# Optimization experiments

Measured on AMD Instinct MI355X. Metric: run time of the kernel, lower is better.

Reference implementation:

```python
import jax, jax.numpy as jnp
import numpy as np

B, N, D = 256, 128, 512
NUM_TYPES, NUM_STATS = 6, 8
W_TYPE, W_STATS, W_CORR = 1.0, 1.0, 0.5
LN_EPS = 1e-5


def setup_inputs() -> dict:
    key = jax.random.key(0)
    ks = jax.random.split(key, 20)
    s = 1.0 / np.sqrt(D)
    inp = {
        "column_embeddings": jax.random.normal(ks[0], (B, N, D), jnp.float32),
        "masked_columns": jax.random.bernoulli(ks[1], 0.15, (B, N)),
        "type_targets": jax.random.randint(ks[2], (N,), 0, NUM_TYPES),
        "column_statistics": jax.random.normal(ks[3], (B, N, NUM_STATS), jnp.float32),
        "column_correlations": jnp.tanh(jax.random.normal(ks[4], (B, N, N), jnp.float32)),
        # type head: Linear(D,D) -> GELU -> LayerNorm -> Linear(D,NUM_TYPES)
        "t_W1": jax.random.normal(ks[5], (D, D), jnp.float32) * s,
        "t_b1": jnp.zeros((D,), jnp.float32),
        "t_g": jnp.ones((D,), jnp.float32),
        "t_beta": jnp.zeros((D,), jnp.float32),
        "t_W2": jax.random.normal(ks[6], (D, NUM_TYPES), jnp.float32) * s,
        "t_b2": jnp.zeros((NUM_TYPES,), jnp.float32),
        # stats head
        "s_W1": jax.random.normal(ks[7], (D, D), jnp.float32) * s,
        "s_b1": jnp.zeros((D,), jnp.float32),
        "s_g": jnp.ones((D,), jnp.float32),
        "s_beta": jnp.zeros((D,), jnp.float32),
        "s_W2": jax.random.normal(ks[8], (D, NUM_STATS), jnp.float32) * s,
        "s_b2": jnp.zeros((NUM_STATS,), jnp.float32),
        # bilinear correlation: x_i^T W x_j + b
        "c_W": jax.random.normal(ks[9], (D, D), jnp.float32) * s,
        "c_b": jnp.zeros((), jnp.float32),
    }
    return inp


def _mlp_head(x, W1, b1, g, beta, W2, b2):
    h = jax.nn.gelu(x @ W1 + b1, approximate=False)
    mu = h.mean(-1, keepdims=True)
    var = ((h - mu) ** 2).mean(-1, keepdims=True)
    h = (h - mu) * jax.lax.rsqrt(var + LN_EPS) * g + beta
    return h @ W2 + b2


def _forward(column_embeddings, masked_columns, type_targets,
             column_statistics, column_correlations,
             t_W1, t_b1, t_g, t_beta, t_W2, t_b2,
             s_W1, s_b1, s_g, s_beta, s_W2, s_b2,
             c_W, c_b):
    e = column_embeddings  # [B,N,D]
    type_logits = _mlp_head(e, t_W1, t_b1, t_g, t_beta, t_W2, t_b2)   # [B,N,T]
    stats_preds = _mlp_head(e, s_W1, s_b1, s_g, s_beta, s_W2, s_b2)   # [B,N,S]

    # batched bilinear correlation: tanh(e_i W e_j + b), diag forced to 1
    u = jnp.einsum('bnd,de->bne', e, c_W)            # [B,N,D]
    corr = jnp.tanh(jnp.einsum('bne,bme->bnm', u, e) + c_b)  # [B,N,N]
    eye = jnp.eye(e.shape[1], dtype=corr.dtype)
    corr = corr * (1.0 - eye) + eye

    m = masked_columns.astype(jnp.float32)           # [B,N]
    n_masked = jnp.maximum(m.sum(), 1.0)

    # type loss: masked-mean cross entropy; targets broadcast over batch
    logp = jax.nn.log_softmax(type_logits, axis=-1)
    tgt = jnp.broadcast_to(type_targets[None, :], m.shape)
    ce = -jnp.take_along_axis(logp, tgt[..., None], axis=-1)[..., 0]  # [B,N]
    type_loss = (ce * m).sum() / n_masked

    # stats loss: masked-mean MSE over [B,N,S]
    se = (stats_preds - column_statistics) ** 2
    stats_loss = (se * m[..., None]).sum() / (n_masked * se.shape[-1])

    # correlation loss: mask_expanded = m_i | m_j
    me = jnp.maximum(m[:, :, None], m[:, None, :])   # [B,N,N]
    n_me = jnp.maximum(me.sum(), 1.0)
    ce2 = (corr - column_correlations) ** 2
    correlation_loss = (ce2 * me).sum() / n_me

    total = W_TYPE * type_loss + W_STATS * stats_loss + W_CORR * correlation_loss
    return total


def reference(column_embeddings, masked_columns, type_targets,
              column_statistics, column_correlations,
              t_W1, t_b1, t_g, t_beta, t_W2, t_b2,
              s_W1, s_b1, s_g, s_beta, s_W2, s_b2,
              c_W, c_b):
    return _forward(column_embeddings, masked_columns, type_targets,
                    column_statistics, column_correlations,
                    t_W1, t_b1, t_g, t_beta, t_W2, t_b2,
                    s_W1, s_b1, s_g, s_beta, s_W2, s_b2,
                    c_W, c_b)
```

## Files before the change

### kernel.cpp

```cpp
#include <hip/hip_runtime.h>
#include <math.h>

#define Bx 256
#define Nx 128
#define Dx 512
#define Mx (Bx * Nx)
#define NTYPES 6
#define NSTATS 8
#define LN_EPS 1e-5f
#define CAP 8192

typedef __attribute__((ext_vector_type(8))) short frag8;
typedef __attribute__((ext_vector_type(4))) float f32x4;

__device__ __forceinline__ unsigned short f2bf(float f) {
    unsigned u = __float_as_uint(f);
    u += 0x7fff + ((u >> 16) & 1);
    return (unsigned short)(u >> 16);
}
__device__ __forceinline__ float bf2f(unsigned short s) {
    return __uint_as_float((unsigned)s << 16);
}

#define ASYNC16(g, l) __builtin_amdgcn_global_load_lds(                      \
    (const __attribute__((address_space(1))) void*)(g),                      \
    (__attribute__((address_space(3))) void*)(l), 16, 0, 0)

#define EB_OFF    0ULL
#define U_OFF     33554432ULL
#define EC_OFF    67108864ULL
#define HC_OFF    75497472ULL
#define WT_OFF    92274688ULL
#define WTC_OFF   93323264ULL
#define LIST_OFF  93847552ULL
#define POS_OFF   93978624ULL
#define CNTS_OFF  94109696ULL
#define PACC_OFF  94110720ULL
#define PCORR_OFF 94112768ULL
#define CNTP_OFF  94113792ULL

__global__ __launch_bounds__(256) void k_prep(
    const float* __restrict__ W0, const float* __restrict__ W1,
    const float* __restrict__ W2, unsigned short* __restrict__ Tcmb,
    unsigned short* __restrict__ Tc, const int* __restrict__ m,
    int* __restrict__ list, int* __restrict__ pos, int* __restrict__ cnts,
    int* cntp) {
    if (blockIdx.x >= 768) {
        const int b = blockIdx.x - 768;
        const int t = threadIdx.x;
        const int r = b * Nx + t;
        int v = 0;
        if (t < 128) v = (m[r] != 0) ? 1 : 0;
        const unsigned long long bal = __ballot(v);
        const int wid = t >> 6, lane = t & 63;
        __shared__ int wcnt[2];
        __shared__ int base;
        if (lane == 0 && wid < 2) wcnt[wid] = __popcll(bal);
        __syncthreads();
        const int cnt = wcnt[0] + wcnt[1];
        if (t == 0) {
            base = atomicAdd(cntp, cnt);
            cnts[b] = cnt;
        }
        __syncthreads();
        if (t < 128) {
            int p = -1;
            if (v) {
                const int rank = __popcll(bal & ((1ULL << lane) - 1)) +
                                 (wid ? wcnt[0] : 0);
                p = base + rank;
                if (p < CAP) list[p] = r;
            }
            pos[r] = (p >= 0 && p < CAP) ? p : -1;
        }
        return;
    }
    const int lin = blockIdx.x * 256 + threadIdx.x;
    const int mid = lin >> 16;
    const int i4  = (lin & 65535) * 4;
    const int n = i4 >> 9, k = i4 & 511;
    const float* W = (mid == 0) ? W0 : (mid == 1) ? W1 : W2;
    unsigned short* T = (mid == 2) ? Tc : (Tcmb + mid * 262144);
    unsigned short o[4];
#pragma unroll
    for (int j = 0; j < 4; ++j) o[j] = f2bf(W[(k + j) * Dx + n]);
    uint2 u;
    u.x = (unsigned)o[0] | ((unsigned)o[1] << 16);
    u.y = (unsigned)o[2] | ((unsigned)o[3] << 16);
    *(uint2*)(T + i4) = u;
}

__global__ __launch_bounds__(256) void k_convE_gather(
    const float* __restrict__ e, const int* __restrict__ pos,
    unsigned short* __restrict__ Eb, unsigned short* __restrict__ Ec) {
    const int r = blockIdx.x * 4 + (threadIdx.x >> 6);
    const int lane = threadIdx.x & 63;
    const int p = pos[r];
    const float4* src = (const float4*)(e + (size_t)r * Dx);
    const float4 a = src[lane * 2];
    const float4 b = src[lane * 2 + 1];
    unsigned short u[8] = {f2bf(a.x), f2bf(a.y), f2bf(a.z), f2bf(a.w),
                           f2bf(b.x), f2bf(b.y), f2bf(b.z), f2bf(b.w)};
    const uint4 v = *(const uint4*)u;
    ((uint4*)(Eb + (size_t)r * Dx))[lane] = v;
    if (p >= 0) ((uint4*)(Ec + (size_t)p * Dx))[lane] = v;
}

__global__ __launch_bounds__(256) void k_gemms(
    const unsigned short* __restrict__ Eb,
    const unsigned short* __restrict__ Ec,
    const unsigned short* __restrict__ Wtc,
    const unsigned short* __restrict__ Wtcmb,
    const float* __restrict__ bias0, const float* __restrict__ bias1,
    unsigned short* __restrict__ U, unsigned short* __restrict__ Hc,
    const int* __restrict__ cntp) {
    __shared__ unsigned short As[128 * 32];
    __shared__ unsigned short Bs[128 * 32];
    const int bid = blockIdx.x;
    const unsigned short *A, *Bt;
    unsigned short* C;
    int row0, col0, ldc, head;
    if (bid < 1024) {
        A = Eb; Bt = Wtc; C = U;
        row0 = (bid >> 2) << 7; col0 = (bid & 3) << 7;
        ldc = 512; head = 0;
    } else {
        const int b2 = bid - 1024;
        row0 = (b2 >> 3) << 7;
        if (row0 >= min(*cntp, CAP)) return;
        col0 = (b2 & 7) << 7;
        A = Ec; Bt = Wtcmb; C = Hc;
        ldc = 1024; head = 1;
    }
    const int t = threadIdx.x;
    const int w = t >> 6, l = t & 63;
    const int wr = (w >> 1) * 64, wcol = (w & 1) * 64;
    const int quad = l >> 4, mr = l & 15;

    const unsigned short* Ag0 = A + (size_t)(row0 + (t >> 2)) * Dx + (t & 3) * 8;
    const unsigned short* Ag1 = Ag0 + (size_t)64 * Dx;
    const unsigned short* Bg0 = Bt + (size_t)(col0 + (t >> 2)) * Dx + (t & 3) * 8;
    const unsigned short* Bg1 = Bg0 + (size_t)64 * Dx;
    unsigned short* Al0 = As + t * 8;
    unsigned short* Al1 = As + (t + 256) * 8;
    unsigned short* Bl0 = Bs + t * 8;
    unsigned short* Bl1 = Bs + (t + 256) * 8;

    f32x4 acc[4][4] = {};
    for (int k0 = 0; k0 < Dx; k0 += 32) {
        __syncthreads();
        ASYNC16(Ag0 + k0, Al0);
        ASYNC16(Ag1 + k0, Al1);
        ASYNC16(Bg0 + k0, Bl0);
        ASYNC16(Bg1 + k0, Bl1);
        __syncthreads();
        frag8 a[4], b[4];
#pragma unroll
        for (int i = 0; i < 4; ++i)
            a[i] = *(const frag8*)&As[(wr + i * 16 + mr) * 32 + quad * 8];
#pragma unroll
        for (int j = 0; j < 4; ++j)
            b[j] = *(const frag8*)&Bs[(wcol + j * 16 + mr) * 32 + quad * 8];
#pragma unroll
        for (int i = 0; i < 4; ++i)
#pragma unroll
            for (int j = 0; j < 4; ++j)
                acc[i][j] = __builtin_amdgcn_mfma_f32_16x16x32_bf16(
                    a[i], b[j], acc[i][j], 0, 0, 0);
    }
#pragma unroll
    for (int i = 0; i < 4; ++i)
#pragma unroll
        for (int j = 0; j < 4; ++j)
#pragma unroll
            for (int r = 0; r < 4; ++r) {
                const int row = row0 + wr + i * 16 + quad * 4 + r;
                const int col = col0 + wcol + j * 16 + mr;
                float v = acc[i][j][r];
                if (head) {
                    v += (col < 512) ? bias0[col] : bias1[col - 512];
                    v = 0.5f * v * (1.0f + erff(v * 0.70710678118654752f));
                }
                C[(size_t)row * ldc + col] = f2bf(v);
            }
}

__global__ __launch_bounds__(256) void k_tail(
    const unsigned short* __restrict__ U,
    const unsigned short* __restrict__ Eb,
    const float* __restrict__ Ct, const int* __restrict__ m,
    const float* __restrict__ cbp, float* __restrict__ pcorr,
    const unsigned short* __restrict__ Hc,
    const float* __restrict__ tg, const float* __restrict__ tbeta,
    const float* __restrict__ tW2, const float* __restrict__ tb2,
    const float* __restrict__ sg, const float* __restrict__ sbeta,
    const float* __restrict__ sW2, const float* __restrict__ sb2,
    const int* __restrict__ list, const int* __restrict__ cntp,
    const int* __restrict__ tgt, const float* __restrict__ stats,
    float* __restrict__ pacc) {
    __shared__ unsigned short As[128 * 32];
    __shared__ unsigned short Bs[128 * 32];
    __shared__ float mloc[128];
    __shared__ float redf[4][2];
    const int t = threadIdx.x;
    const int w = t >> 6, l = t & 63;

    if (blockIdx.x < 256) {
        const int b = blockIdx.x;
        const int wr = (w >> 1) * 64, wcol = (w & 1) * 64;
        const int quad = l >> 4, mr = l & 15;
        if (t < 128) mloc[t] = (m[b * Nx + t] != 0) ? 1.0f : 0.0f;

        const unsigned short* Ub = U + (size_t)b * Nx * Dx;
        const unsigned short* E  = Eb + (size_t)b * Nx * Dx;
        const unsigned short* Ag0 = Ub + (size_t)(t >> 2) * Dx + (t & 3) * 8;
        const unsigned short* Ag1 = Ag0 + (size_t)64 * Dx;
        const unsigned short* Bg0 = E + (size_t)(t >> 2) * Dx + (t & 3) * 8;
        const unsigned short* Bg1 = Bg0 + (size_t)64 * Dx;
        unsigned short* Al0 = As + t * 8;
        unsigned short* Al1 = As + (t + 256) * 8;
        unsigned short* Bl0 = Bs + t * 8;
        unsigned short* Bl1 = Bs + (t + 256) * 8;

        f32x4 acc_r[4][4] = {};
        for (int k0 = 0; k0 < Dx; k0 += 32) {
            __syncthreads();
            ASYNC16(Ag0 + k0, Al0);
            ASYNC16(Ag1 + k0, Al1);
            ASYNC16(Bg0 + k0, Bl0);
            ASYNC16(Bg1 + k0, Bl1);
            __syncthreads();
            frag8 a[4], bfr[4];
#pragma unroll
            for (int i = 0; i < 4; ++i)
                a[i] = *(const frag8*)&As[(wr + i * 16 + mr) * 32 + quad * 8];
#pragma unroll
            for (int j = 0; j < 4; ++j)
                bfr[j] = *(const frag8*)&Bs[(wcol + j * 16 + mr) * 32 + quad * 8];
#pragma unroll
            for (int i = 0; i < 4; ++i)
#pragma unroll
                for (int j = 0; j < 4; ++j)
                    acc_r[i][j] = __builtin_amdgcn_mfma_f32_16x16x32_bf16(
                        a[i], bfr[j], acc_r[i][j], 0, 0, 0);
        }
        const float cb = cbp[0];
        float lsum = 0.0f;
#pragma unroll
        for (int i = 0; i < 4; ++i)
#pragma unroll
            for (int j = 0; j < 4; ++j)
#pragma unroll
                for (int r = 0; r < 4; ++r) {
                    const int row = wr + i * 16 + quad * 4 + r;
                    const int col = wcol + j * 16 + mr;
                    float c = (row == col) ? 1.0f : tanhf(acc_r[i][j][r] + cb);
                    const float me = fmaxf(mloc[row], mloc[col]);
                    const float d = c - Ct[((size_t)b * Nx + row) * Nx + col];
                    lsum += me * d * d;
                }
#pragma unroll
        for (int off = 32; off > 0; off >>= 1) lsum += __shfl_down(lsum, off);
        if (l == 0) redf[w][0] = lsum;
        __syncthreads();
        if (t == 0) pcorr[b] = redf[0][0] + redf[1][0] + redf[2][0] + redf[3][0];
        return;
    }

    const int blk = blockIdx.x - 256;
    const int cnt = min(*cntp, CAP);
    float ce_acc = 0.0f, sse_acc = 0.0f;
    for (int idx = blk * 4 + w; idx < cnt; idx += 256 * 4) {
        const int r = list[idx];
        const uint4 ut = ((const uint4*)(Hc + (size_t)idx * 1024))[l];
        const uint4 us = ((const uint4*)(Hc + (size_t)idx * 1024 + 512))[l];
        float a[8], b8[8];
        {
            const unsigned uu[4] = {ut.x, ut.y, ut.z, ut.w};
            const unsigned vv[4] = {us.x, us.y, us.z, us.w};
#pragma unroll
            for (int j = 0; j < 4; ++j) {
                a[2 * j]      = bf2f((unsigned short)(uu[j] & 0xffff));
                a[2 * j + 1]  = bf2f((unsigned short)(uu[j] >> 16));
                b8[2 * j]     = bf2f((unsigned short)(vv[j] & 0xffff));
                b8[2 * j + 1] = bf2f((unsigned short)(vv[j] >> 16));
            }
        }
        float st = 0, qt = 0, ss = 0, qs = 0;
#pragma unroll
        for (int j = 0; j < 8; ++j) {
            st += a[j]; qt += a[j] * a[j];
            ss += b8[j]; qs += b8[j] * b8[j];
        }
#pragma unroll
        for (int off = 32; off > 0; off >>= 1) {
            st += __shfl_xor(st, off); qt += __shfl_xor(qt, off);
            ss += __shfl_xor(ss, off); qs += __shfl_xor(qs, off);
        }
        const float mt = st * (1.0f / Dx);
        const float rt = rsqrtf(qt * (1.0f / Dx) - mt * mt + LN_EPS);
        const float ms = ss * (1.0f / Dx);
        const float rs = rsqrtf(qs * (1.0f / Dx) - ms * ms + LN_EPS);

        const int c0 = l * 8;
        float tp[6] = {}, sp[8] = {};
#pragma unroll
        for (int j = 0; j < 8; ++j) {
            const int c = c0 + j;
            const float nt = (a[j] - mt) * rt * tg[c] + tbeta[c];
#pragma unroll
            for (int k = 0; k < 6; ++k) tp[k] += nt * tW2[c * 6 + k];
            const float ns = (b8[j] - ms) * rs * sg[c] + sbeta[c];
#pragma unroll
            for (int k = 0; k < 8; ++k) sp[k] += ns * sW2[c * 8 + k];
        }
#pragma unroll
        for (int k = 0; k < 6; ++k)
#pragma unroll
            for (int off = 32; off > 0; off >>= 1) tp[k] += __shfl_down(tp[k], off);
#pragma unroll
        for (int k = 0; k < 8; ++k)
#pragma unroll
            for (int off = 32; off > 0; off >>= 1) sp[k] += __shfl_down(sp[k], off);

        if (l == 0) {
            float lg[6];
#pragma unroll
            for (int k = 0; k < 6; ++k) lg[k] = tp[k] + tb2[k];
            float mx = lg[0];
#pragma unroll
            for (int k = 1; k < 6; ++k) mx = fmaxf(mx, lg[k]);
            float se = 0.0f;
#pragma unroll
            for (int k = 0; k < 6; ++k) se += expf(lg[k] - mx);
            ce_acc += -(lg[tgt[r & (Nx - 1)]] - mx - logf(se));
            float sse = 0.0f;
#pragma unroll
            for (int k = 0; k < 8; ++k) {
                const float d = sp[k] + sb2[k] - stats[(size_t)r * NSTATS + k];
                sse += d * d;
            }
            sse_acc += sse;
        }
    }
    if (l == 0) { redf[w][0] = ce_acc; redf[w][1] = sse_acc; }
    __syncthreads();
    if (t == 0) {
        pacc[2 * blk]     = redf[0][0] + redf[1][0] + redf[2][0] + redf[3][0];
        pacc[2 * blk + 1] = redf[0][1] + redf[1][1] + redf[2][1] + redf[3][1];
    }
}

__global__ __launch_bounds__(256) void k_final(
    const float* __restrict__ pacc, const float* __restrict__ pcorr,
    const int* __restrict__ cnts, const int* __restrict__ cntp,
    float* __restrict__ out) {
    const int t = threadIdx.x, w = t >> 6, lane = t & 63;
    float ce = pacc[2 * t], sse = pacc[2 * t + 1], co = pcorr[t];
    const int c = cnts[t];
    float me = (float)(Nx * Nx) - (float)((Nx - c) * (Nx - c));
#pragma unroll
    for (int off = 32; off > 0; off >>= 1) {
        ce += __shfl_down(ce, off);
        sse += __shfl_down(sse, off);
        co += __shfl_down(co, off);
        me += __shfl_down(me, off);
    }
    __shared__ float red[4][4];
    if (lane == 0) {
        red[w][0] = ce; red[w][1] = sse; red[w][2] = co; red[w][3] = me;
    }
    __syncthreads();
    if (t == 0) {
        const float CE = red[0][0] + red[1][0] + red[2][0] + red[3][0];
        const float SSE = red[0][1] + red[1][1] + red[2][1] + red[3][1];
        const float CO = red[0][2] + red[1][2] + red[2][2] + red[3][2];
        const float ME = red[0][3] + red[1][3] + red[2][3] + red[3][3];
        const float nm = fmaxf((float)*cntp, 1.0f);
        const float nme = fmaxf(ME, 1.0f);
        out[0] = CE / nm + SSE / (nm * (float)NSTATS) + 0.5f * CO / nme;
    }
}

extern "C" void kernel_launch(void* const* d_in, const int* in_sizes, int n_in,
                              void* d_out, int out_size, void* d_ws, size_t ws_size,
                              hipStream_t stream) {
    const float* e      = (const float*)d_in[0];
    const int*   mcols  = (const int*)d_in[1];
    const int*   ttgt   = (const int*)d_in[2];
    const float* stats  = (const float*)d_in[3];
    const float* corrT  = (const float*)d_in[4];
    const float* tW1    = (const float*)d_in[5];
    const float* tb1    = (const float*)d_in[6];
    const float* tg     = (const float*)d_in[7];
    const float* tbeta  = (const float*)d_in[8];
    const float* tW2    = (const float*)d_in[9];
    const float* tb2    = (const float*)d_in[10];
    const float* sW1    = (const float*)d_in[11];
    const float* sb1    = (const float*)d_in[12];
    const float* sg     = (const float*)d_in[13];
    const float* sbeta  = (const float*)d_in[14];
    const float* sW2    = (const float*)d_in[15];
    const float* sb2    = (const float*)d_in[16];
    const float* cW     = (const float*)d_in[17];
    const float* cb     = (const float*)d_in[18];
    float* out = (float*)d_out;

    char* ws = (char*)d_ws;
    unsigned short* Eb    = (unsigned short*)(ws + EB_OFF);
    unsigned short* U     = (unsigned short*)(ws + U_OFF);
    unsigned short* Ec    = (unsigned short*)(ws + EC_OFF);
    unsigned short* Hc    = (unsigned short*)(ws + HC_OFF);
    unsigned short* Wtcmb = (unsigned short*)(ws + WT_OFF);
    unsigned short* Wtc   = (unsigned short*)(ws + WTC_OFF);
    int*   list  = (int*)(ws + LIST_OFF);
    int*   pos   = (int*)(ws + POS_OFF);
    int*   cnts  = (int*)(ws + CNTS_OFF);
    float* pacc  = (float*)(ws + PACC_OFF);
    float* pcorr = (float*)(ws + PCORR_OFF);
    int*   cntp  = (int*)(ws + CNTP_OFF);

    hipMemsetAsync(cntp, 0, sizeof(int), stream);
    k_prep<<<1024, 256, 0, stream>>>(tW1, sW1, cW, Wtcmb, Wtc, mcols,
                                     list, pos, cnts, cntp);
    k_convE_gather<<<Mx / 4, 256, 0, stream>>>(e, pos, Eb, Ec);
    k_gemms<<<1536, 256, 0, stream>>>(Eb, Ec, Wtc, Wtcmb, tb1, sb1, U, Hc, cntp);
    k_tail<<<512, 256, 0, stream>>>(U, Eb, corrT, mcols, cb, pcorr,
                                    Hc, tg, tbeta, tW2, tb2, sg, sbeta, sW2, sb2,
                                    list, cntp, ttgt, stats, pacc);
    k_final<<<1, 256, 0, stream>>>(pacc, pcorr, cnts, cntp, out);
}
```

Baseline: 254.1 us.

## Fuse E conversion into prep, gather masked rows in GEMM, double K-step

```diff
diff --git a/kernel.cpp b/kernel.cpp
--- a/kernel.cpp
+++ b/kernel.cpp
@@ -28,26 +28,25 @@
 
 #define EB_OFF    0ULL
 #define U_OFF     33554432ULL
-#define EC_OFF    67108864ULL
-#define HC_OFF    75497472ULL
-#define WT_OFF    92274688ULL
-#define WTC_OFF   93323264ULL
-#define LIST_OFF  93847552ULL
-#define POS_OFF   93978624ULL
-#define CNTS_OFF  94109696ULL
-#define PACC_OFF  94110720ULL
-#define PCORR_OFF 94112768ULL
-#define CNTP_OFF  94113792ULL
+#define HC_OFF    67108864ULL
+#define WT_OFF    83886080ULL
+#define WTC_OFF   84934656ULL
+#define LIST_OFF  85458944ULL
+#define CNTS_OFF  85590016ULL
+#define PACC_OFF  85591040ULL
+#define PCORR_OFF 85593088ULL
+#define CNTP_OFF  85594112ULL
 
 __global__ __launch_bounds__(256) void k_prep(
-    const float* __restrict__ W0, const float* __restrict__ W1,
-    const float* __restrict__ W2, unsigned short* __restrict__ Tcmb,
+    const float* __restrict__ e, const float* __restrict__ W0,
+    const float* __restrict__ W1, const float* __restrict__ W2,
+    unsigned short* __restrict__ Eb, unsigned short* __restrict__ Tcmb,
     unsigned short* __restrict__ Tc, const int* __restrict__ m,
-    int* __restrict__ list, int* __restrict__ pos, int* __restrict__ cnts,
-    int* cntp) {
-    if (blockIdx.x >= 768) {
-        const int b = blockIdx.x - 768;
-        const int t = threadIdx.x;
+    int* __restrict__ list, int* __restrict__ cnts, int* cntp) {
+    const int bid = blockIdx.x;
+    const int t = threadIdx.x;
+    if (bid < 256) {
+        const int b = bid;
         const int r = b * Nx + t;
         int v = 0;
         if (t < 128) v = (m[r] != 0) ? 1 : 0;
@@ -63,110 +62,106 @@
             cnts[b] = cnt;
         }
         __syncthreads();
-        if (t < 128) {
-            int p = -1;
-            if (v) {
-                const int rank = __popcll(bal & ((1ULL << lane) - 1)) +
-                                 (wid ? wcnt[0] : 0);
-                p = base + rank;
-                if (p < CAP) list[p] = r;
-            }
-            pos[r] = (p >= 0 && p < CAP) ? p : -1;
+        if (t < 128 && v) {
+            const int rank = __popcll(bal & ((1ULL << lane) - 1)) +
+                             (wid ? wcnt[0] : 0);
+            const int p = base + rank;
+            if (p < CAP) list[p] = r;
         }
         return;
     }
-    const int lin = blockIdx.x * 256 + threadIdx.x;
-    const int mid = lin >> 16;
-    const int i4  = (lin & 65535) * 4;
-    const int n = i4 >> 9, k = i4 & 511;
-    const float* W = (mid == 0) ? W0 : (mid == 1) ? W1 : W2;
-    unsigned short* T = (mid == 2) ? Tc : (Tcmb + mid * 262144);
-    unsigned short o[4];
-#pragma unroll
-    for (int j = 0; j < 4; ++j) o[j] = f2bf(W[(k + j) * Dx + n]);
-    uint2 u;
-    u.x = (unsigned)o[0] | ((unsigned)o[1] << 16);
-    u.y = (unsigned)o[2] | ((unsigned)o[3] << 16);
-    *(uint2*)(T + i4) = u;
-}
-
-__global__ __launch_bounds__(256) void k_convE_gather(
-    const float* __restrict__ e, const int* __restrict__ pos,
-    unsigned short* __restrict__ Eb, unsigned short* __restrict__ Ec) {
-    const int r = blockIdx.x * 4 + (threadIdx.x >> 6);
-    const int lane = threadIdx.x & 63;
-    const int p = pos[r];
+    if (bid < 1024) {
+        const int lin = (bid - 256) * 256 + t;
+        const int mid = lin >> 16;
+        const int i4  = (lin & 65535) * 4;
+        const int n = i4 >> 9, k = i4 & 511;
+        const float* W = (mid == 0) ? W0 : (mid == 1) ? W1 : W2;
+        unsigned short* T = (mid == 2) ? Tc : (Tcmb + mid * 262144);
+        unsigned short o[4];
+#pragma unroll
+        for (int j = 0; j < 4; ++j) o[j] = f2bf(W[(k + j) * Dx + n]);
+        uint2 u;
+        u.x = (unsigned)o[0] | ((unsigned)o[1] << 16);
+        u.y = (unsigned)o[2] | ((unsigned)o[3] << 16);
+        *(uint2*)(T + i4) = u;
+        return;
+    }
+    const int r = (bid - 1024) * 4 + (t >> 6);
+    const int lane = t & 63;
     const float4* src = (const float4*)(e + (size_t)r * Dx);
     const float4 a = src[lane * 2];
     const float4 b = src[lane * 2 + 1];
     unsigned short u[8] = {f2bf(a.x), f2bf(a.y), f2bf(a.z), f2bf(a.w),
                            f2bf(b.x), f2bf(b.y), f2bf(b.z), f2bf(b.w)};
-    const uint4 v = *(const uint4*)u;
-    ((uint4*)(Eb + (size_t)r * Dx))[lane] = v;
-    if (p >= 0) ((uint4*)(Ec + (size_t)p * Dx))[lane] = v;
+    ((uint4*)(Eb + (size_t)r * Dx))[lane] = *(const uint4*)u;
 }
 
 __global__ __launch_bounds__(256) void k_gemms(
     const unsigned short* __restrict__ Eb,
-    const unsigned short* __restrict__ Ec,
     const unsigned short* __restrict__ Wtc,
     const unsigned short* __restrict__ Wtcmb,
     const float* __restrict__ bias0, const float* __restrict__ bias1,
     unsigned short* __restrict__ U, unsigned short* __restrict__ Hc,
-    const int* __restrict__ cntp) {
-    __shared__ unsigned short As[128 * 32];
-    __shared__ unsigned short Bs[128 * 32];
+    const int* __restrict__ list, const int* __restrict__ cntp) {
+    __shared__ unsigned short As[2 * 4096];
+    __shared__ unsigned short Bs[2 * 4096];
     const int bid = blockIdx.x;
-    const unsigned short *A, *Bt;
+    const int t = threadIdx.x;
+    const unsigned short* Bt;
     unsigned short* C;
-    int row0, col0, ldc, head;
+    int row0, col0, ldc, head, ra0, ra1;
     if (bid < 1024) {
-        A = Eb; Bt = Wtc; C = U;
-        row0 = (bid >> 2) << 7; col0 = (bid & 3) << 7;
-        ldc = 512; head = 0;
+        row0 = ((((bid >> 5) << 3) | (bid & 7))) << 7;
+        col0 = ((bid >> 3) & 3) << 7;
+        Bt = Wtc; C = U; ldc = 512; head = 0;
+        ra0 = row0 + (t >> 2);
+        ra1 = ra0 + 64;
     } else {
         const int b2 = bid - 1024;
         row0 = (b2 >> 3) << 7;
-        if (row0 >= min(*cntp, CAP)) return;
+        const int cnt = min(*cntp, CAP);
+        if (row0 >= cnt) return;
         col0 = (b2 & 7) << 7;
-        A = Ec; Bt = Wtcmb; C = Hc;
-        ldc = 1024; head = 1;
-    }
-    const int t = threadIdx.x;
+        Bt = Wtcmb; C = Hc; ldc = 1024; head = 1;
+        ra0 = list[min(row0 + (t >> 2), cnt - 1)];
+        ra1 = list[min(row0 + 64 + (t >> 2), cnt - 1)];
+    }
     const int w = t >> 6, l = t & 63;
     const int wr = (w >> 1) * 64, wcol = (w & 1) * 64;
     const int quad = l >> 4, mr = l & 15;
 
-    const unsigned short* Ag0 = A + (size_t)(row0 + (t >> 2)) * Dx + (t & 3) * 8;
-    const unsigned short* Ag1 = Ag0 + (size_t)64 * Dx;
+    const unsigned short* Ag0 = Eb + (size_t)ra0 * Dx + (t & 3) * 8;
+    const unsigned short* Ag1 = Eb + (size_t)ra1 * Dx + (t & 3) * 8;
     const unsigned short* Bg0 = Bt + (size_t)(col0 + (t >> 2)) * Dx + (t & 3) * 8;
     const unsigned short* Bg1 = Bg0 + (size_t)64 * Dx;
-    unsigned short* Al0 = As + t * 8;
-    unsigned short* Al1 = As + (t + 256) * 8;
-    unsigned short* Bl0 = Bs + t * 8;
-    unsigned short* Bl1 = Bs + (t + 256) * 8;
 
     f32x4 acc[4][4] = {};
-    for (int k0 = 0; k0 < Dx; k0 += 32) {
+    for (int k0 = 0; k0 < Dx; k0 += 64) {
         __syncthreads();
-        ASYNC16(Ag0 + k0, Al0);
-        ASYNC16(Ag1 + k0, Al1);
-        ASYNC16(Bg0 + k0, Bl0);
-        ASYNC16(Bg1 + k0, Bl1);
+#pragma unroll
+        for (int s = 0; s < 2; ++s) {
+            ASYNC16(Ag0 + k0 + s * 32, As + s * 4096 + t * 8);
+            ASYNC16(Ag1 + k0 + s * 32, As + s * 4096 + (t + 256) * 8);
+            ASYNC16(Bg0 + k0 + s * 32, Bs + s * 4096 + t * 8);
+            ASYNC16(Bg1 + k0 + s * 32, Bs + s * 4096 + (t + 256) * 8);
+        }
         __syncthreads();
-        frag8 a[4], b[4];
-#pragma unroll
-        for (int i = 0; i < 4; ++i)
-            a[i] = *(const frag8*)&As[(wr + i * 16 + mr) * 32 + quad * 8];
-#pragma unroll
-        for (int j = 0; j < 4; ++j)
-            b[j] = *(const frag8*)&Bs[(wcol + j * 16 + mr) * 32 + quad * 8];
-#pragma unroll
-        for (int i = 0; i < 4; ++i)
+#pragma unroll
+        for (int s = 0; s < 2; ++s) {
+            frag8 a[4], b[4];
+#pragma unroll
+            for (int i = 0; i < 4; ++i)
+                a[i] = *(const frag8*)&As[s * 4096 + (wr + i * 16 + mr) * 32 + quad * 8];
 #pragma unroll
             for (int j = 0; j < 4; ++j)
-                acc[i][j] = __builtin_amdgcn_mfma_f32_16x16x32_bf16(
-                    a[i], b[j], acc[i][j], 0, 0, 0);
+                b[j] = *(const frag8*)&Bs[s * 4096 + (wcol + j * 16 + mr) * 32 + quad * 8];
+#pragma unroll
+            for (int i = 0; i < 4; ++i)
+#pragma unroll
+                for (int j = 0; j < 4; ++j)
+                    acc[i][j] = __builtin_amdgcn_mfma_f32_16x16x32_bf16(
+                        a[i], b[j], acc[i][j], 0, 0, 0);
+        }
     }
 #pragma unroll
     for (int i = 0; i < 4; ++i)
@@ -198,8 +193,8 @@
     const int* __restrict__ list, const int* __restrict__ cntp,
     const int* __restrict__ tgt, const float* __restrict__ stats,
     float* __restrict__ pacc) {
-    __shared__ unsigned short As[128 * 32];
-    __shared__ unsigned short Bs[128 * 32];
+    __shared__ unsigned short As[2 * 4096];
+    __shared__ unsigned short Bs[2 * 4096];
     __shared__ float mloc[128];
     __shared__ float redf[4][2];
     const int t = threadIdx.x;
@@ -217,32 +212,34 @@
         const unsigned short* Ag1 = Ag0 + (size_t)64 * Dx;
         const unsigned short* Bg0 = E + (size_t)(t >> 2) * Dx + (t & 3) * 8;
         const unsigned short* Bg1 = Bg0 + (size_t)64 * Dx;
-        unsigned short* Al0 = As + t * 8;
-        unsigned short* Al1 = As + (t + 256) * 8;
-        unsigned short* Bl0 = Bs + t * 8;
-        unsigned short* Bl1 = Bs + (t + 256) * 8;
 
         f32x4 acc_r[4][4] = {};
-        for (int k0 = 0; k0 < Dx; k0 += 32) {
+        for (int k0 = 0; k0 < Dx; k0 += 64) {
             __syncthreads();
-            ASYNC16(Ag0 + k0, Al0);
-            ASYNC16(Ag1 + k0, Al1);
-            ASYNC16(Bg0 + k0, Bl0);
-            ASYNC16(Bg1 + k0, Bl1);
+#pragma unroll
+            for (int s = 0; s < 2; ++s) {
+                ASYNC16(Ag0 + k0 + s * 32, As + s * 4096 + t * 8);
+                ASYNC16(Ag1 + k0 + s * 32, As + s * 4096 + (t + 256) * 8);
+                ASYNC16(Bg0 + k0 + s * 32, Bs + s * 4096 + t * 8);
+                ASYNC16(Bg1 + k0 + s * 32, Bs + s * 4096 + (t + 256) * 8);
+            }
             __syncthreads();
-            frag8 a[4], bfr[4];
-#pragma unroll
-            for (int i = 0; i < 4; ++i)
-                a[i] = *(const frag8*)&As[(wr + i * 16 + mr) * 32 + quad * 8];
-#pragma unroll
-            for (int j = 0; j < 4; ++j)
-                bfr[j] = *(const frag8*)&Bs[(wcol + j * 16 + mr) * 32 + quad * 8];
-#pragma unroll
-            for (int i = 0; i < 4; ++i)
+#pragma unroll
+            for (int s = 0; s < 2; ++s) {
+                frag8 a[4], bfr[4];
+#pragma unroll
+                for (int i = 0; i < 4; ++i)
+                    a[i] = *(const frag8*)&As[s * 4096 + (wr + i * 16 + mr) * 32 + quad * 8];
 #pragma unroll
                 for (int j = 0; j < 4; ++j)
-                    acc_r[i][j] = __builtin_amdgcn_mfma_f32_16x16x32_bf16(
-                        a[i], bfr[j], acc_r[i][j], 0, 0, 0);
+                    bfr[j] = *(const frag8*)&Bs[s * 4096 + (wcol + j * 16 + mr) * 32 + quad * 8];
+#pragma unroll
+                for (int i = 0; i < 4; ++i)
+#pragma unroll
+                    for (int j = 0; j < 4; ++j)
+                        acc_r[i][j] = __builtin_amdgcn_mfma_f32_16x16x32_bf16(
+                            a[i], bfr[j], acc_r[i][j], 0, 0, 0);
+            }
         }
         const float cb = cbp[0];
         float lsum = 0.0f;
@@ -409,22 +406,19 @@
     char* ws = (char*)d_ws;
     unsigned short* Eb    = (unsigned short*)(ws + EB_OFF);
     unsigned short* U     = (unsigned short*)(ws + U_OFF);
-    unsigned short* Ec    = (unsigned short*)(ws + EC_OFF);
     unsigned short* Hc    = (unsigned short*)(ws + HC_OFF);
     unsigned short* Wtcmb = (unsigned short*)(ws + WT_OFF);
     unsigned short* Wtc   = (unsigned short*)(ws + WTC_OFF);
     int*   list  = (int*)(ws + LIST_OFF);
-    int*   pos   = (int*)(ws + POS_OFF);
     int*   cnts  = (int*)(ws + CNTS_OFF);
     float* pacc  = (float*)(ws + PACC_OFF);
     float* pcorr = (float*)(ws + PCORR_OFF);
     int*   cntp  = (int*)(ws + CNTP_OFF);
 
     hipMemsetAsync(cntp, 0, sizeof(int), stream);
-    k_prep<<<1024, 256, 0, stream>>>(tW1, sW1, cW, Wtcmb, Wtc, mcols,
-                                     list, pos, cnts, cntp);
-    k_convE_gather<<<Mx / 4, 256, 0, stream>>>(e, pos, Eb, Ec);
-    k_gemms<<<1536, 256, 0, stream>>>(Eb, Ec, Wtc, Wtcmb, tb1, sb1, U, Hc, cntp);
+    k_prep<<<9216, 256, 0, stream>>>(e, tW1, sW1, cW, Eb, Wtcmb, Wtc, mcols,
+                                     list, cnts, cntp);
+    k_gemms<<<1536, 256, 0, stream>>>(Eb, Wtc, Wtcmb, tb1, sb1, U, Hc, list, cntp);
     k_tail<<<512, 256, 0, stream>>>(U, Eb, corrT, mcols, cb, pcorr,
                                     Hc, tg, tbeta, tW2, tb2, sg, sbeta, sW2, sb2,
                                     list, cntp, ttgt, stats, pacc);
```

Result: faster. 240.4 us (-5.4%).
